# Performance work log

Measured on AMD Instinct MI355X. Metric: run time of the kernel, lower is better.

Reference implementation:

```python
import jax, jax.numpy as jnp
import numpy as np

N, M, E, C_IN, C_OUT = 100000, 20000, 1600000, 128, 128


def _safe_inv(d):
    # 1/d with 0 where d==0 (matches PyG D[D==inf]=0), grad-safe
    safe = jnp.where(d > 0, d, 1.0)
    return jnp.where(d > 0, 1.0 / safe, 0.0)


def _hconv(x, node_idx, edge_idx, hw, W, b):
    # PyG HypergraphConv, use_attention=False, heads=1:
    # X' = D^{-1} H B^{-1} H^T (X Theta) + bias, D uses hyperedge_weight
    xt = x @ W  # [N, C_OUT]
    D = jax.ops.segment_sum(hw[edge_idx], node_idx, num_segments=N)
    Dinv = _safe_inv(D)  # [N]
    Bc = jax.ops.segment_sum(jnp.ones((E,), dtype=x.dtype), edge_idx, num_segments=M)
    Binv = _safe_inv(Bc)  # [M]
    # node -> hyperedge (message weighted by B^{-1} of target edge)
    e = jax.ops.segment_sum(Binv[edge_idx][:, None] * xt[node_idx], edge_idx, num_segments=M)
    # hyperedge -> node (message weighted by D^{-1} of target node)
    out = jax.ops.segment_sum(Dinv[node_idx][:, None] * e[edge_idx], node_idx, num_segments=N)
    return out + b


def setup_inputs() -> dict:
    key = jax.random.key(0)
    ks = jax.random.split(key, 12)
    x = jax.random.normal(ks[0], (N, C_IN), dtype=jnp.float32)
    node_idx = jax.random.randint(ks[1], (E,), 0, N, dtype=jnp.int32)
    edge_idx = jax.random.randint(ks[2], (E,), 0, M, dtype=jnp.int32)
    hyperedge_index = jnp.stack([node_idx, edge_idx])
    hyperedge_weight = jax.random.uniform(ks[3], (M,), dtype=jnp.float32) + 0.5
    hyperedge_attr = jax.random.normal(ks[4], (M, C_IN), dtype=jnp.float32)
    batch = jnp.zeros((N,), dtype=jnp.int32)
    s1 = 1.0 / np.sqrt(C_IN)
    s2 = 1.0 / np.sqrt(C_OUT)
    W1 = jax.random.uniform(ks[5], (C_IN, C_OUT), minval=-s1, maxval=s1, dtype=jnp.float32)
    W2 = jax.random.uniform(ks[6], (C_OUT, C_OUT), minval=-s2, maxval=s2, dtype=jnp.float32)
    W3 = jax.random.uniform(ks[7], (C_OUT, C_OUT), minval=-s2, maxval=s2, dtype=jnp.float32)
    b1 = jax.random.uniform(ks[8], (C_OUT,), minval=-s1, maxval=s1, dtype=jnp.float32)
    b2 = jax.random.uniform(ks[9], (C_OUT,), minval=-s2, maxval=s2, dtype=jnp.float32)
    b3 = jax.random.uniform(ks[10], (C_OUT,), minval=-s2, maxval=s2, dtype=jnp.float32)
    return {"x": x, "hyperedge_index": hyperedge_index, "hyperedge_weight": hyperedge_weight,
            "hyperedge_attr": hyperedge_attr, "batch": batch,
            "W1": W1, "b1": b1, "W2": W2, "b2": b2, "W3": W3, "b3": b3}


def reference(x, hyperedge_index, hyperedge_weight, hyperedge_attr, batch,
              W1, b1, W2, b2, W3, b3):
    node_idx = hyperedge_index[0]
    edge_idx = hyperedge_index[1]
    # dropout is identity in eval mode; hyperedge_attr/batch unused (no attention)
    h = jax.nn.relu(_hconv(x, node_idx, edge_idx, hyperedge_weight, W1, b1))
    h = jax.nn.relu(_hconv(h, node_idx, edge_idx, hyperedge_weight, W2, b2))
    h = jax.nn.relu(_hconv(h, node_idx, edge_idx, hyperedge_weight, W3, b3))
    return h
```

## Files before the change

kernel.cpp:

```cpp
#include <hip/hip_runtime.h>
#include <hip/hip_fp16.h>

#define NN 100000
#define MM 20000
#define EE 1600000

#define NBLK_E 256
#define CHUNK_E (EE / NBLK_E)
#define NBLK_N 128
#define CHUNK_N (EE / NBLK_N)
#define NRANGE_U8 50000
#define FN_PASSES 8
#define FN_RANGE (NN / FN_PASSES)
#define FILL_NODE_BLOCKS (FN_PASSES * NBLK_N)
#define DINV_BLOCKS ((NN + 255) / 256)
#define CVT_BLOCKS 1024

#define SCAN_BLOCK 256
#define SCAN_ITEMS 8
#define SCAN_TILE (SCAN_BLOCK * SCAN_ITEMS)
#define NB_E ((MM + SCAN_TILE - 1) / SCAN_TILE)
#define NB_N ((NN + SCAN_TILE - 1) / SCAN_TILE)
#define NB_TOT (NB_E + NB_N)

static inline size_t align256(size_t x) { return (x + 255) & ~(size_t)255; }

struct alignas(8) half4 { __half2 lo, hi; };

__device__ __forceinline__ float4 h4_to_f4(half4 v) {
  float2 a = __half22float2(v.lo);
  float2 b = __half22float2(v.hi);
  return make_float4(a.x, a.y, b.x, b.y);
}
__device__ __forceinline__ half4 f4_to_h4(float4 v) {
  half4 r;
  r.lo = __float22half2_rn(make_float2(v.x, v.y));
  r.hi = __float22half2_rn(make_float2(v.z, v.w));
  return r;
}

__global__ __launch_bounds__(256) void hist_kernel(
    const int* __restrict__ node_idx, const int* __restrict__ edge_idx,
    unsigned short* __restrict__ bcnt_e, unsigned short* __restrict__ lrank_e,
    unsigned short* __restrict__ bcnt_n, unsigned short* __restrict__ lrank_n) {
  extern __shared__ unsigned int smem[];
  if (blockIdx.x < NBLK_E) {
    int b = blockIdx.x;
    for (int k = threadIdx.x; k < MM / 2; k += 256) smem[k] = 0;
    __syncthreads();
    int lo = b * CHUNK_E, hi = lo + CHUNK_E;
    for (int i = lo + threadIdx.x; i < hi; i += 256) {
      int e = edge_idx[i];
      unsigned add = (e & 1) ? 0x10000u : 1u;
      unsigned old = atomicAdd(&smem[e >> 1], add);
      lrank_e[i] = (unsigned short)((old >> ((e & 1) * 16)) & 0xFFFFu);
    }
    __syncthreads();
    unsigned short* row = bcnt_e + (size_t)b * MM;
    for (int k = threadIdx.x; k < MM / 2; k += 256) {
      unsigned w = smem[k];
      ushort2 o;
      o.x = (unsigned short)(w & 0xFFFFu);
      o.y = (unsigned short)(w >> 16);
      ((ushort2*)row)[k] = o;
    }
  } else {
    int b = blockIdx.x - NBLK_E;
    int lo = b * CHUNK_N, hi = lo + CHUNK_N;
    unsigned short* row = bcnt_n + (size_t)b * NN;
    for (int p = 0; p < 2; ++p) {
      int base = p * NRANGE_U8;
      for (int k = threadIdx.x; k < NRANGE_U8 / 4; k += 256) smem[k] = 0;
      __syncthreads();
      for (int i = lo + threadIdx.x; i < hi; i += 256) {
        int n = node_idx[i] - base;
        if ((unsigned)n < (unsigned)NRANGE_U8) {
          unsigned sh = (n & 3) * 8;
          unsigned old = atomicAdd(&smem[n >> 2], 1u << sh);
          lrank_n[i] = (unsigned short)((old >> sh) & 0xFFu);
        }
      }
      __syncthreads();
      for (int k = threadIdx.x; k < NRANGE_U8 / 4; k += 256) {
        unsigned w = smem[k];
        ushort4 o;
        o.x = (unsigned short)(w & 0xFFu);
        o.y = (unsigned short)((w >> 8) & 0xFFu);
        o.z = (unsigned short)((w >> 16) & 0xFFu);
        o.w = (unsigned short)((w >> 24) & 0xFFu);
        ((ushort4*)(row + base))[k] = o;
      }
      __syncthreads();
    }
  }
}

__global__ __launch_bounds__(256) void colscan_kernel(
    unsigned short* __restrict__ bcnt_e, unsigned short* __restrict__ bcnt_n,
    int* __restrict__ ecnt, int* __restrict__ ncnt) {
  int i = blockIdx.x * 256 + threadIdx.x;
  if (i < MM) {
    int run = 0;
#pragma unroll 8
    for (int b = 0; b < NBLK_E; ++b) {
      size_t idx = (size_t)b * MM + i;
      int v = bcnt_e[idx];
      bcnt_e[idx] = (unsigned short)run;
      run += v;
    }
    ecnt[i] = run;
  } else if (i < MM + NN) {
    int n = i - MM;
    int run = 0;
#pragma unroll 8
    for (int b = 0; b < NBLK_N; ++b) {
      size_t idx = (size_t)b * NN + n;
      int v = bcnt_n[idx];
      bcnt_n[idx] = (unsigned short)run;
      run += v;
    }
    ncnt[n] = run;
  }
}

__global__ __launch_bounds__(SCAN_BLOCK) void scan_partial_kernel(
    const int* __restrict__ ecnt, const int* __restrict__ ncnt,
    int* __restrict__ eptr, int* __restrict__ nptr, int* __restrict__ bsum) {
  __shared__ int lds[SCAN_BLOCK];
  int b = blockIdx.x;
  const int* cnt; int* ptr; int len; int lb;
  if (b < NB_E) { cnt = ecnt; ptr = eptr; len = MM; lb = b; }
  else          { cnt = ncnt; ptr = nptr; len = NN; lb = b - NB_E; }
  int t = threadIdx.x;
  int lo = lb * SCAN_TILE + t * SCAN_ITEMS;
  int v[SCAN_ITEMS];
  int s = 0;
#pragma unroll
  for (int j = 0; j < SCAN_ITEMS; ++j) {
    int idx = lo + j;
    v[j] = (idx < len) ? cnt[idx] : 0;
    s += v[j];
  }
  lds[t] = s;
  __syncthreads();
  for (int d = 1; d < SCAN_BLOCK; d <<= 1) {
    int o = (t >= d) ? lds[t - d] : 0;
    __syncthreads();
    lds[t] += o;
    __syncthreads();
  }
  int run = lds[t] - s;
#pragma unroll
  for (int j = 0; j < SCAN_ITEMS; ++j) {
    int idx = lo + j;
    if (idx < len) ptr[idx] = run;
    run += v[j];
  }
  if (t == SCAN_BLOCK - 1) bsum[b] = lds[t];
}

__global__ void scan_bsum_kernel(int* __restrict__ bsum) {
  int t = threadIdx.x;
  if (t == 0) {
    int run = 0;
    for (int i = 0; i < NB_E; ++i) { int c = bsum[i]; bsum[i] = run; run += c; }
  } else if (t == 1) {
    int run = 0;
    for (int i = NB_E; i < NB_TOT; ++i) { int c = bsum[i]; bsum[i] = run; run += c; }
  }
}

__global__ __launch_bounds__(SCAN_BLOCK) void scan_fixup_kernel(
    int* __restrict__ eptr, int* __restrict__ nptr,
    const int* __restrict__ ecnt, const int* __restrict__ bsum,
    float* __restrict__ Binv) {
  int b = blockIdx.x;
  int* ptr; int len; int lb; bool isE;
  if (b < NB_E) { ptr = eptr; len = MM; lb = b; isE = true; }
  else          { ptr = nptr; len = NN; lb = b - NB_E; isE = false; }
  int boff = bsum[b];
  int t = threadIdx.x;
  int lo = lb * SCAN_TILE + t * SCAN_ITEMS;
#pragma unroll
  for (int j = 0; j < SCAN_ITEMS; ++j) {
    int idx = lo + j;
    if (idx < len) {
      ptr[idx] += boff;
      if (isE) {
        int c = ecnt[idx];
        Binv[idx] = (c > 0) ? 1.0f / (float)c : 0.0f;
      }
    }
  }
  if (b == 0 && t == 0) { eptr[MM] = EE; nptr[NN] = EE; }
}

__global__ __launch_bounds__(256) void fill_kernel(
    const int* __restrict__ node_idx, const int* __restrict__ edge_idx,
    const int* __restrict__ eptr, const int* __restrict__ nptr,
    const unsigned short* __restrict__ bcnt_e,
    const unsigned short* __restrict__ bcnt_n,
    const unsigned short* __restrict__ lrank_e,
    const unsigned short* __restrict__ lrank_n,
    int* __restrict__ edge_nodes, int* __restrict__ node_edges) {
  extern __shared__ unsigned short srow[];
  if (blockIdx.x < NBLK_E) {
    int b = blockIdx.x;
    const unsigned short* src = bcnt_e + (size_t)b * MM;
    for (int k = threadIdx.x; k < MM / 2; k += 256)
      ((ushort2*)srow)[k] = ((const ushort2*)src)[k];
    __syncthreads();
    int lo = b * CHUNK_E, hi = lo + CHUNK_E;
    for (int i = lo + threadIdx.x; i < hi; i += 256) {
      int e = edge_idx[i];
      int slot = eptr[e] + (int)srow[e] + (int)lrank_e[i];
      edge_nodes[slot] = node_idx[i];
    }
  } else {
    int bid = blockIdx.x - NBLK_E;
    int p = bid / NBLK_N;
    int b = bid % NBLK_N;
    int base = p * FN_RANGE;
    const unsigned short* row = bcnt_n + (size_t)b * NN + base;
    for (int k = threadIdx.x; k < FN_RANGE / 2; k += 256)
      ((ushort2*)srow)[k] = ((const ushort2*)row)[k];
    __syncthreads();
    int lo = b * CHUNK_N, hi = lo + CHUNK_N;
    for (int i = lo + threadIdx.x; i < hi; i += 256) {
      int n = node_idx[i] - base;
      if ((unsigned)n < (unsigned)FN_RANGE) {
        int slot = nptr[n + base] + (int)srow[n] + (int)lrank_n[i];
        node_edges[slot] = edge_idx[i];
      }
    }
  }
}

__global__ __launch_bounds__(256) void dinv_cvt_kernel(
    const int* __restrict__ nptr, const int* __restrict__ node_edges,
    const float* __restrict__ hw, float* __restrict__ Dinv,
    const float* __restrict__ x, __half* __restrict__ xh) {
  if (blockIdx.x < DINV_BLOCKS) {
    int n = blockIdx.x * 256 + threadIdx.x;
    if (n >= NN) return;
    int lo = nptr[n], hi = nptr[n + 1];
    float d = 0.0f;
    for (int j = lo; j < hi; ++j) d += hw[node_edges[j]];
    Dinv[n] = (d > 0.0f) ? 1.0f / d : 0.0f;
  } else {
    int i = (blockIdx.x - DINV_BLOCKS) * 256 + threadIdx.x;
    int stride = CVT_BLOCKS * 256;
    for (; i < NN * 32; i += stride) {
      float4 v = ((const float4*)x)[i];
      ((half4*)xh)[i] = f4_to_h4(v);
    }
  }
}

__device__ __forceinline__ void fma4(float4& acc, float s, const float4& m) {
  acc.x += s * m.x;
  acc.y += s * m.y;
  acc.z += s * m.z;
  acc.w += s * m.w;
}

__global__ __launch_bounds__(256) void gemm128_kernel(
    const __half* __restrict__ X, const float* __restrict__ W,
    __half* __restrict__ Y, int nrows) {
  __shared__ float Wl[128 * 128];
  float4* Wl4 = (float4*)Wl;
  const float4* W4 = (const float4*)W;
  for (int i = threadIdx.x; i < 128 * 32; i += 256) Wl4[i] = W4[i];
  __syncthreads();

  int tc = threadIdx.x & 15;
  int tr = threadIdx.x >> 4;
  int base = blockIdx.x * 64;
  int r[4];
  bool v[4];
#pragma unroll
  for (int j = 0; j < 4; ++j) {
    int rr = base + tr + j * 16;
    v[j] = rr < nrows;
    r[j] = v[j] ? rr : 0;
  }
  float4 acc[4][2];
#pragma unroll
  for (int j = 0; j < 4; ++j) {
    acc[j][0] = make_float4(0.f, 0.f, 0.f, 0.f);
    acc[j][1] = make_float4(0.f, 0.f, 0.f, 0.f);
  }
#pragma unroll 4
  for (int k4 = 0; k4 < 32; ++k4) {
    float4 xv[4];
#pragma unroll
    for (int j = 0; j < 4; ++j)
      xv[j] = h4_to_f4(((const half4*)X)[(size_t)r[j] * 32 + k4]);
#pragma unroll
    for (int kk = 0; kk < 4; ++kk) {
      float4 wva = Wl4[(k4 * 4 + kk) * 32 + tc];
      float4 wvb = Wl4[(k4 * 4 + kk) * 32 + 16 + tc];
#pragma unroll
      for (int j = 0; j < 4; ++j) {
        float xk = ((const float*)&xv[j])[kk];
        fma4(acc[j][0], xk, wva);
        fma4(acc[j][1], xk, wvb);
      }
    }
  }
#pragma unroll
  for (int j = 0; j < 4; ++j) {
    if (v[j]) {
      ((half4*)Y)[(size_t)r[j] * 32 + tc] = f4_to_h4(acc[j][0]);
      ((half4*)Y)[(size_t)r[j] * 32 + 16 + tc] = f4_to_h4(acc[j][1]);
    }
  }
}

__global__ __launch_bounds__(256) void edge_agg_kernel(
    const __half* __restrict__ hin, const int* __restrict__ eptr,
    const int* __restrict__ edge_nodes, const float* __restrict__ Binv,
    __half* __restrict__ eout) {
  int half_id = threadIdx.x >> 5;
  int lane = threadIdx.x & 31;
  int m = blockIdx.x * 8 + half_id;
  if (m >= MM) return;
  int lo = eptr[m], hi = eptr[m + 1];
  const half4* h4p = (const half4*)hin;
  float4 acc = make_float4(0.f, 0.f, 0.f, 0.f);
  int j = lo;
  for (; j + 8 <= hi; j += 8) {
    int idx[8];
#pragma unroll
    for (int u = 0; u < 8; ++u) idx[u] = edge_nodes[j + u];
    float4 s[8];
#pragma unroll
    for (int u = 0; u < 8; ++u) s[u] = h4_to_f4(h4p[(size_t)idx[u] * 32 + lane]);
    acc.x += ((s[0].x + s[1].x) + (s[2].x + s[3].x)) + ((s[4].x + s[5].x) + (s[6].x + s[7].x));
    acc.y += ((s[0].y + s[1].y) + (s[2].y + s[3].y)) + ((s[4].y + s[5].y) + (s[6].y + s[7].y));
    acc.z += ((s[0].z + s[1].z) + (s[2].z + s[3].z)) + ((s[4].z + s[5].z) + (s[6].z + s[7].z));
    acc.w += ((s[0].w + s[1].w) + (s[2].w + s[3].w)) + ((s[4].w + s[5].w) + (s[6].w + s[7].w));
  }
  for (; j < hi; ++j) {
    int n = edge_nodes[j];
    float4 a = h4_to_f4(h4p[(size_t)n * 32 + lane]);
    acc.x += a.x; acc.y += a.y; acc.z += a.z; acc.w += a.w;
  }
  float bi = Binv[m];
  acc.x *= bi; acc.y *= bi; acc.z *= bi; acc.w *= bi;
  ((half4*)eout)[(size_t)m * 32 + lane] = f4_to_h4(acc);
}

__device__ __forceinline__ void strow(float* Y, size_t i, float4 v) {
  ((float4*)Y)[i] = v;
}
__device__ __forceinline__ void strow(__half* Y, size_t i, float4 v) {
  ((half4*)Y)[i] = f4_to_h4(v);
}

template <typename TOUT>
__global__ __launch_bounds__(256) void node_agg_kernel(
    const __half* __restrict__ ein, const int* __restrict__ nptr,
    const int* __restrict__ node_edges, const float* __restrict__ Dinv,
    const float* __restrict__ bias, TOUT* __restrict__ out) {
  int half_id = threadIdx.x >> 5;
  int lane = threadIdx.x & 31;
  int n = blockIdx.x * 8 + half_id;
  if (n >= NN) return;
  int lo = nptr[n], hi = nptr[n + 1];
  const half4* e4 = (const half4*)ein;
  float4 acc = make_float4(0.f, 0.f, 0.f, 0.f);
  int j = lo;
  for (; j + 4 <= hi; j += 4) {
    int m0 = node_edges[j + 0];
    int m1 = node_edges[j + 1];
    int m2 = node_edges[j + 2];
    int m3 = node_edges[j + 3];
    float4 a = h4_to_f4(e4[(size_t)m0 * 32 + lane]);
    float4 b = h4_to_f4(e4[(size_t)m1 * 32 + lane]);
    float4 c = h4_to_f4(e4[(size_t)m2 * 32 + lane]);
    float4 d = h4_to_f4(e4[(size_t)m3 * 32 + lane]);
    acc.x += (a.x + b.x) + (c.x + d.x);
    acc.y += (a.y + b.y) + (c.y + d.y);
    acc.z += (a.z + b.z) + (c.z + d.z);
    acc.w += (a.w + b.w) + (c.w + d.w);
  }
  for (; j < hi; ++j) {
    int m = node_edges[j];
    float4 a = h4_to_f4(e4[(size_t)m * 32 + lane]);
    acc.x += a.x; acc.y += a.y; acc.z += a.z; acc.w += a.w;
  }
  float di = Dinv[n];
  float4 bb = ((const float4*)bias)[lane];
  float4 rv;
  rv.x = fmaxf(di * acc.x + bb.x, 0.f);
  rv.y = fmaxf(di * acc.y + bb.y, 0.f);
  rv.z = fmaxf(di * acc.z + bb.z, 0.f);
  rv.w = fmaxf(di * acc.w + bb.w, 0.f);
  strow(out, (size_t)n * 32 + lane, rv);
}

extern "C" void kernel_launch(void* const* d_in, const int* in_sizes, int n_in,
                              void* d_out, int out_size, void* d_ws, size_t ws_size,
                              hipStream_t stream) {
  const float* x = (const float*)d_in[0];
  const int* hidx = (const int*)d_in[1];
  const int* node_idx = hidx;
  const int* edge_idx = hidx + EE;
  const float* hw = (const float*)d_in[2];
  const float* W1 = (const float*)d_in[5];
  const float* b1 = (const float*)d_in[6];
  const float* W2 = (const float*)d_in[7];
  const float* b2 = (const float*)d_in[8];
  const float* W3 = (const float*)d_in[9];
  const float* b3 = (const float*)d_in[10];
  float* out = (float*)d_out;

  char* ws = (char*)d_ws;
  size_t off = 0;
  auto alloc = [&](size_t bytes) -> char* {
    char* p = ws + off;
    off = align256(off + bytes);
    return p;
  };
  __half* xh   = (__half*)alloc(sizeof(__half) * (size_t)NN * 128);
  __half* h    = (__half*)alloc(sizeof(__half) * (size_t)NN * 128);
  __half* eraw = (__half*)alloc(sizeof(__half) * (size_t)MM * 128);
  __half* et   = (__half*)alloc(sizeof(__half) * (size_t)MM * 128);
  unsigned short* bcnt_e = (unsigned short*)alloc(sizeof(short) * (size_t)NBLK_E * MM);
  unsigned short* bcnt_n = (unsigned short*)alloc(sizeof(short) * (size_t)NBLK_N * NN);
  unsigned short* lrank_e = (unsigned short*)alloc(sizeof(short) * (size_t)EE);
  unsigned short* lrank_n = (unsigned short*)alloc(sizeof(short) * (size_t)EE);
  int*   ecnt  = (int*)alloc(sizeof(int) * MM);
  int*   ncnt  = (int*)alloc(sizeof(int) * NN);
  int*   eptr  = (int*)alloc(sizeof(int) * (MM + 1));
  int*   nptr  = (int*)alloc(sizeof(int) * (NN + 1));
  int*   bsum  = (int*)alloc(sizeof(int) * NB_TOT);
  float* Binv  = (float*)alloc(sizeof(float) * MM);
  float* Dinv  = (float*)alloc(sizeof(float) * NN);
  int* edge_nodes = (int*)alloc(sizeof(int) * (size_t)EE);
  int* node_edges = (int*)alloc(sizeof(int) * (size_t)EE);
  (void)ws_size; (void)in_sizes; (void)n_in; (void)out_size;

  hist_kernel<<<NBLK_E + NBLK_N, 256, (NRANGE_U8 / 4) * sizeof(int), stream>>>(
      node_idx, edge_idx, bcnt_e, lrank_e, bcnt_n, lrank_n);
  colscan_kernel<<<(MM + NN + 255) / 256, 256, 0, stream>>>(bcnt_e, bcnt_n, ecnt, ncnt);
  scan_partial_kernel<<<NB_TOT, SCAN_BLOCK, 0, stream>>>(ecnt, ncnt, eptr, nptr, bsum);
  scan_bsum_kernel<<<1, 64, 0, stream>>>(bsum);
  scan_fixup_kernel<<<NB_TOT, SCAN_BLOCK, 0, stream>>>(eptr, nptr, ecnt, bsum, Binv);
  fill_kernel<<<NBLK_E + FILL_NODE_BLOCKS, 256, MM * sizeof(short), stream>>>(
      node_idx, edge_idx, eptr, nptr, bcnt_e, bcnt_n, lrank_e, lrank_n,
      edge_nodes, node_edges);
  dinv_cvt_kernel<<<DINV_BLOCKS + CVT_BLOCKS, 256, 0, stream>>>(
      nptr, node_edges, hw, Dinv, x, xh);

  const int gemmE_grid = (MM + 63) / 64;
  const int eagg_grid = MM / 8;
  const int nagg_grid = NN / 8;

  edge_agg_kernel<<<eagg_grid, 256, 0, stream>>>(xh, eptr, edge_nodes, Binv, eraw);
  gemm128_kernel<<<gemmE_grid, 256, 0, stream>>>(eraw, W1, et, MM);
  node_agg_kernel<__half><<<nagg_grid, 256, 0, stream>>>(et, nptr, node_edges, Dinv, b1, h);
  edge_agg_kernel<<<eagg_grid, 256, 0, stream>>>(h, eptr, edge_nodes, Binv, eraw);
  gemm128_kernel<<<gemmE_grid, 256, 0, stream>>>(eraw, W2, et, MM);
  node_agg_kernel<__half><<<nagg_grid, 256, 0, stream>>>(et, nptr, node_edges, Dinv, b2, xh);
  edge_agg_kernel<<<eagg_grid, 256, 0, stream>>>(xh, eptr, edge_nodes, Binv, eraw);
  gemm128_kernel<<<gemmE_grid, 256, 0, stream>>>(eraw, W3, et, MM);
  node_agg_kernel<float><<<nagg_grid, 256, 0, stream>>>(et, nptr, node_edges, Dinv, b3, out);
}
```

Baseline: 555.6 us.

## Fuse edge aggregation with per-edge GEMM and move x conversion into hist

Each edge-aggregation warp now multiplies its aggregated 128-vector by W directly, using shuffles and an fp16 copy of W in shared memory. This removes the separate GEMM launch and the eraw round trip through memory. The x fp32→fp16 conversion moves into the histogram kernel so it overlaps with the setup work, and the fill kernel's node-block index mapping is interleaved. The costs are a reload and convert of W in every block (2500 blocks), heavy use of shuffles, and W rounded to fp16.

```diff
diff --git a/kernel.cpp b/kernel.cpp
--- a/kernel.cpp
+++ b/kernel.cpp
@@ -39,10 +39,11 @@
   return r;
 }
 
-__global__ __launch_bounds__(256) void hist_kernel(
+__global__ __launch_bounds__(256) void hist_cvt_kernel(
     const int* __restrict__ node_idx, const int* __restrict__ edge_idx,
     unsigned short* __restrict__ bcnt_e, unsigned short* __restrict__ lrank_e,
-    unsigned short* __restrict__ bcnt_n, unsigned short* __restrict__ lrank_n) {
+    unsigned short* __restrict__ bcnt_n, unsigned short* __restrict__ lrank_n,
+    const float* __restrict__ x, __half* __restrict__ xh) {
   extern __shared__ unsigned int smem[];
   if (blockIdx.x < NBLK_E) {
     int b = blockIdx.x;
@@ -64,7 +65,7 @@
       o.y = (unsigned short)(w >> 16);
       ((ushort2*)row)[k] = o;
     }
-  } else {
+  } else if (blockIdx.x < NBLK_E + NBLK_N) {
     int b = blockIdx.x - NBLK_E;
     int lo = b * CHUNK_N, hi = lo + CHUNK_N;
     unsigned short* row = bcnt_n + (size_t)b * NN;
@@ -92,6 +93,13 @@
       }
       __syncthreads();
     }
+  } else {
+    int i = (blockIdx.x - NBLK_E - NBLK_N) * 256 + threadIdx.x;
+    int stride = CVT_BLOCKS * 256;
+    for (; i < NN * 32; i += stride) {
+      float4 v = ((const float4*)x)[i];
+      ((half4*)xh)[i] = f4_to_h4(v);
+    }
   }
 }
 
@@ -218,8 +226,8 @@
     }
   } else {
     int bid = blockIdx.x - NBLK_E;
-    int p = bid / NBLK_N;
-    int b = bid % NBLK_N;
+    int p = bid & 7;
+    int b = bid >> 3;
     int base = p * FN_RANGE;
     const unsigned short* row = bcnt_n + (size_t)b * NN + base;
     for (int k = threadIdx.x; k < FN_RANGE / 2; k += 256)
@@ -236,25 +244,15 @@
   }
 }
 
-__global__ __launch_bounds__(256) void dinv_cvt_kernel(
+__global__ __launch_bounds__(256) void dinv_kernel(
     const int* __restrict__ nptr, const int* __restrict__ node_edges,
-    const float* __restrict__ hw, float* __restrict__ Dinv,
-    const float* __restrict__ x, __half* __restrict__ xh) {
-  if (blockIdx.x < DINV_BLOCKS) {
-    int n = blockIdx.x * 256 + threadIdx.x;
-    if (n >= NN) return;
-    int lo = nptr[n], hi = nptr[n + 1];
-    float d = 0.0f;
-    for (int j = lo; j < hi; ++j) d += hw[node_edges[j]];
-    Dinv[n] = (d > 0.0f) ? 1.0f / d : 0.0f;
-  } else {
-    int i = (blockIdx.x - DINV_BLOCKS) * 256 + threadIdx.x;
-    int stride = CVT_BLOCKS * 256;
-    for (; i < NN * 32; i += stride) {
-      float4 v = ((const float4*)x)[i];
-      ((half4*)xh)[i] = f4_to_h4(v);
-    }
-  }
+    const float* __restrict__ hw, float* __restrict__ Dinv) {
+  int n = blockIdx.x * 256 + threadIdx.x;
+  if (n >= NN) return;
+  int lo = nptr[n], hi = nptr[n + 1];
+  float d = 0.0f;
+  for (int j = lo; j < hi; ++j) d += hw[node_edges[j]];
+  Dinv[n] = (d > 0.0f) ? 1.0f / d : 0.0f;
 }
 
 __device__ __forceinline__ void fma4(float4& acc, float s, const float4& m) {
@@ -264,67 +262,20 @@
   acc.w += s * m.w;
 }
 
-__global__ __launch_bounds__(256) void gemm128_kernel(
-    const __half* __restrict__ X, const float* __restrict__ W,
-    __half* __restrict__ Y, int nrows) {
-  __shared__ float Wl[128 * 128];
-  float4* Wl4 = (float4*)Wl;
-  const float4* W4 = (const float4*)W;
-  for (int i = threadIdx.x; i < 128 * 32; i += 256) Wl4[i] = W4[i];
-  __syncthreads();
-
-  int tc = threadIdx.x & 15;
-  int tr = threadIdx.x >> 4;
-  int base = blockIdx.x * 64;
-  int r[4];
-  bool v[4];
-#pragma unroll
-  for (int j = 0; j < 4; ++j) {
-    int rr = base + tr + j * 16;
-    v[j] = rr < nrows;
-    r[j] = v[j] ? rr : 0;
-  }
-  float4 acc[4][2];
-#pragma unroll
-  for (int j = 0; j < 4; ++j) {
-    acc[j][0] = make_float4(0.f, 0.f, 0.f, 0.f);
-    acc[j][1] = make_float4(0.f, 0.f, 0.f, 0.f);
-  }
-#pragma unroll 4
-  for (int k4 = 0; k4 < 32; ++k4) {
-    float4 xv[4];
-#pragma unroll
-    for (int j = 0; j < 4; ++j)
-      xv[j] = h4_to_f4(((const half4*)X)[(size_t)r[j] * 32 + k4]);
-#pragma unroll
-    for (int kk = 0; kk < 4; ++kk) {
-      float4 wva = Wl4[(k4 * 4 + kk) * 32 + tc];
-      float4 wvb = Wl4[(k4 * 4 + kk) * 32 + 16 + tc];
-#pragma unroll
-      for (int j = 0; j < 4; ++j) {
-        float xk = ((const float*)&xv[j])[kk];
-        fma4(acc[j][0], xk, wva);
-        fma4(acc[j][1], xk, wvb);
-      }
-    }
-  }
-#pragma unroll
-  for (int j = 0; j < 4; ++j) {
-    if (v[j]) {
-      ((half4*)Y)[(size_t)r[j] * 32 + tc] = f4_to_h4(acc[j][0]);
-      ((half4*)Y)[(size_t)r[j] * 32 + 16 + tc] = f4_to_h4(acc[j][1]);
-    }
-  }
-}
-
-__global__ __launch_bounds__(256) void edge_agg_kernel(
+__global__ __launch_bounds__(256) void eagg_gemm_kernel(
     const __half* __restrict__ hin, const int* __restrict__ eptr,
     const int* __restrict__ edge_nodes, const float* __restrict__ Binv,
-    __half* __restrict__ eout) {
+    const float* __restrict__ W, __half* __restrict__ et) {
+  __shared__ half4 Wl[128 * 32];
+  for (int i = threadIdx.x; i < 128 * 32; i += 256) {
+    float4 w = ((const float4*)W)[i];
+    Wl[i] = f4_to_h4(w);
+  }
+  __syncthreads();
+
   int half_id = threadIdx.x >> 5;
   int lane = threadIdx.x & 31;
   int m = blockIdx.x * 8 + half_id;
-  if (m >= MM) return;
   int lo = eptr[m], hi = eptr[m + 1];
   const half4* h4p = (const half4*)hin;
   float4 acc = make_float4(0.f, 0.f, 0.f, 0.f);
@@ -348,7 +299,25 @@
   }
   float bi = Binv[m];
   acc.x *= bi; acc.y *= bi; acc.z *= bi; acc.w *= bi;
-  ((half4*)eout)[(size_t)m * 32 + lane] = f4_to_h4(acc);
+
+  float4 outv = make_float4(0.f, 0.f, 0.f, 0.f);
+#pragma unroll 8
+  for (int sl = 0; sl < 32; ++sl) {
+    float4 r;
+    r.x = __shfl(acc.x, sl, 32);
+    r.y = __shfl(acc.y, sl, 32);
+    r.z = __shfl(acc.z, sl, 32);
+    r.w = __shfl(acc.w, sl, 32);
+    float4 w0 = h4_to_f4(Wl[(4 * sl + 0) * 32 + lane]);
+    float4 w1 = h4_to_f4(Wl[(4 * sl + 1) * 32 + lane]);
+    float4 w2 = h4_to_f4(Wl[(4 * sl + 2) * 32 + lane]);
+    float4 w3 = h4_to_f4(Wl[(4 * sl + 3) * 32 + lane]);
+    fma4(outv, r.x, w0);
+    fma4(outv, r.y, w1);
+    fma4(outv, r.z, w2);
+    fma4(outv, r.w, w3);
+  }
+  ((half4*)et)[(size_t)m * 32 + lane] = f4_to_h4(outv);
 }
 
 __device__ __forceinline__ void strow(float* Y, size_t i, float4 v) {
@@ -425,7 +394,6 @@
   };
   __half* xh   = (__half*)alloc(sizeof(__half) * (size_t)NN * 128);
   __half* h    = (__half*)alloc(sizeof(__half) * (size_t)NN * 128);
-  __half* eraw = (__half*)alloc(sizeof(__half) * (size_t)MM * 128);
   __half* et   = (__half*)alloc(sizeof(__half) * (size_t)MM * 128);
   unsigned short* bcnt_e = (unsigned short*)alloc(sizeof(short) * (size_t)NBLK_E * MM);
   unsigned short* bcnt_n = (unsigned short*)alloc(sizeof(short) * (size_t)NBLK_N * NN);
@@ -442,8 +410,9 @@
   int* node_edges = (int*)alloc(sizeof(int) * (size_t)EE);
   (void)ws_size; (void)in_sizes; (void)n_in; (void)out_size;
 
-  hist_kernel<<<NBLK_E + NBLK_N, 256, (NRANGE_U8 / 4) * sizeof(int), stream>>>(
-      node_idx, edge_idx, bcnt_e, lrank_e, bcnt_n, lrank_n);
+  hist_cvt_kernel<<<NBLK_E + NBLK_N + CVT_BLOCKS, 256,
+                    (NRANGE_U8 / 4) * sizeof(int), stream>>>(
+      node_idx, edge_idx, bcnt_e, lrank_e, bcnt_n, lrank_n, x, xh);
   colscan_kernel<<<(MM + NN + 255) / 256, 256, 0, stream>>>(bcnt_e, bcnt_n, ecnt, ncnt);
   scan_partial_kernel<<<NB_TOT, SCAN_BLOCK, 0, stream>>>(ecnt, ncnt, eptr, nptr, bsum);
   scan_bsum_kernel<<<1, 64, 0, stream>>>(bsum);
@@ -451,20 +420,15 @@
   fill_kernel<<<NBLK_E + FILL_NODE_BLOCKS, 256, MM * sizeof(short), stream>>>(
       node_idx, edge_idx, eptr, nptr, bcnt_e, bcnt_n, lrank_e, lrank_n,
       edge_nodes, node_edges);
-  dinv_cvt_kernel<<<DINV_BLOCKS + CVT_BLOCKS, 256, 0, stream>>>(
-      nptr, node_edges, hw, Dinv, x, xh);
-
-  const int gemmE_grid = (MM + 63) / 64;
+  dinv_kernel<<<DINV_BLOCKS, 256, 0, stream>>>(nptr, node_edges, hw, Dinv);
+
   const int eagg_grid = MM / 8;
   const int nagg_grid = NN / 8;
 
-  edge_agg_kernel<<<eagg_grid, 256, 0, stream>>>(xh, eptr, edge_nodes, Binv, eraw);
-  gemm128_kernel<<<gemmE_grid, 256, 0, stream>>>(eraw, W1, et, MM);
+  eagg_gemm_kernel<<<eagg_grid, 256, 0, stream>>>(xh, eptr, edge_nodes, Binv, W1, et);
   node_agg_kernel<__half><<<nagg_grid, 256, 0, stream>>>(et, nptr, node_edges, Dinv, b1, h);
-  edge_agg_kernel<<<eagg_grid, 256, 0, stream>>>(h, eptr, edge_nodes, Binv, eraw);
-  gemm128_kernel<<<gemmE_grid, 256, 0, stream>>>(eraw, W2, et, MM);
+  eagg_gemm_kernel<<<eagg_grid, 256, 0, stream>>>(h, eptr, edge_nodes, Binv, W2, et);
   node_agg_kernel<__half><<<nagg_grid, 256, 0, stream>>>(et, nptr, node_edges, Dinv, b2, xh);
-  edge_agg_kernel<<<eagg_grid, 256, 0, stream>>>(xh, eptr, edge_nodes, Binv, eraw);
-  gemm128_kernel<<<gemmE_grid, 256, 0, stream>>>(eraw, W3, et, MM);
+  eagg_gemm_kernel<<<eagg_grid, 256, 0, stream>>>(xh, eptr, edge_nodes, Binv, W3, et);
   node_agg_kernel<float><<<nagg_grid, 256, 0, stream>>>(et, nptr, node_edges, Dinv, b3, out);
 }
```

After: 561.5 us. About the same (+1.1%).
